# Performance work log

Measured on AMD Instinct MI355X. Metric: run time of the kernel, lower is better.

The kernel has to match this reference:

```python
import jax, jax.numpy as jnp
import numpy as np

N_NODES = 100000
N_EDGES = 3200000
N_FEAT = 128
N_GRAPHS = 256
N_CLASSES = 10


def setup_inputs() -> dict:
    key = jax.random.key(0)
    ks = jax.random.split(key, 10)
    x = jax.random.normal(ks[0], (N_NODES, N_FEAT), dtype=jnp.float32)
    edge_index = jax.random.randint(ks[1], (2, N_EDGES), 0, N_NODES, dtype=jnp.int64)
    batch = jnp.sort(jax.random.randint(ks[2], (N_NODES,), 0, N_GRAPHS, dtype=jnp.int64))
    # GCNConv weights (glorot-ish scaling) and biases
    W1 = jax.random.normal(ks[3], (N_FEAT, 16), dtype=jnp.float32) / np.sqrt(N_FEAT)
    b1 = jnp.zeros((16,), dtype=jnp.float32)
    W2 = jax.random.normal(ks[4], (16, 32), dtype=jnp.float32) / np.sqrt(16.0)
    b2 = jnp.zeros((32,), dtype=jnp.float32)
    Wfc = jax.random.normal(ks[5], (32, N_CLASSES), dtype=jnp.float32) / np.sqrt(32.0)
    bfc = jnp.zeros((N_CLASSES,), dtype=jnp.float32)
    return {"x": x, "edge_index": edge_index, "batch": batch,
            "W1": W1, "b1": b1, "W2": W2, "b2": b2, "Wfc": Wfc, "bfc": bfc}


def reference(x, edge_index, batch, W1, b1, W2, b2, Wfc, bfc):
    N = x.shape[0]
    # --- GCN normalization with self-loops (PyG GCNConv default) ---
    loop = jnp.arange(N, dtype=edge_index.dtype)
    src = jnp.concatenate([edge_index[0], loop])  # [E+N]
    dst = jnp.concatenate([edge_index[1], loop])  # [E+N]
    ones = jnp.ones_like(src, dtype=x.dtype)
    deg = jax.ops.segment_sum(ones, dst, num_segments=N)  # in-degree incl self-loop
    dinv = jax.lax.rsqrt(deg)  # deg >= 1 thanks to self-loops
    norm = dinv[src] * dinv[dst]  # [E+N]

    def gcn_conv(h, W, b):
        h = h @ W                               # [N, out] linear first (small out dim)
        msg = h[src] * norm[:, None]            # gather + edge-wise scale
        agg = jax.ops.segment_sum(msg, dst, num_segments=N)  # scatter-add
        return agg + b

    h = jax.nn.relu(gcn_conv(x, W1, b1))
    h = jax.nn.relu(gcn_conv(h, W2, b2))

    # --- global mean pool over graphs ---
    g_sum = jax.ops.segment_sum(h, batch, num_segments=N_GRAPHS)  # [G, 32]
    g_cnt = jax.ops.segment_sum(jnp.ones((N,), dtype=h.dtype), batch, num_segments=N_GRAPHS)
    pooled = g_sum / jnp.maximum(g_cnt, 1.0)[:, None]

    return pooled @ Wfc + bfc  # [G, num_classes]
```

## Files before the change

kernel.cpp:

```cpp
#include <hip/hip_runtime.h>
#include <hip/hip_fp16.h>

#define NF   128
#define C1   16
#define C2   32
#define NCLS 10
#define BSH  8
#define BN   256
#define MAXB 512
#define S    9216
#define TILE 4096
#define CAP  12288


__global__ __launch_bounds__(512) void k_bin(const int* __restrict__ ei,
                                             int* __restrict__ packed,
                                             int* __restrict__ offmat,
                                             int E, int nbuck) {
    __shared__ int hist[MAXB];
    __shared__ int off0[MAXB];
    __shared__ int cur[MAXB];
    int tid = threadIdx.x;
    long long t0 = (long long)blockIdx.x * TILE;

    for (int i = tid; i < MAXB; i += 512) hist[i] = 0;
    __syncthreads();

    long long eb = t0 + (long long)tid * 8;
    int src[8], dst[8];
    if (eb + 8 <= E) {
        const int4* s4 = (const int4*)(ei + eb);
        const int4* d4 = (const int4*)(ei + E + eb);
        int4 a = s4[0], b = s4[1], c = d4[0], d = d4[1];
        src[0]=a.x; src[1]=a.y; src[2]=a.z; src[3]=a.w;
        src[4]=b.x; src[5]=b.y; src[6]=b.z; src[7]=b.w;
        dst[0]=c.x; dst[1]=c.y; dst[2]=c.z; dst[3]=c.w;
        dst[4]=d.x; dst[5]=d.y; dst[6]=d.z; dst[7]=d.w;
    } else {
#pragma unroll
        for (int u = 0; u < 8; ++u) {
            long long e = eb + u;
            src[u] = (e < E) ? ei[e] : 0;
            dst[u] = (e < E) ? ei[E + e] : -1;
        }
    }
#pragma unroll
    for (int u = 0; u < 8; ++u)
        if (dst[u] >= 0) atomicAdd(&hist[dst[u] >> BSH], 1);
    __syncthreads();
    if (tid < 64) {
        int carry = 0;
        for (int c = 0; c < MAXB / 64; ++c) {
            int idx = c * 64 + tid;
            int v = hist[idx];
            int orig = v;
            for (int off = 1; off < 64; off <<= 1) {
                int t = __shfl_up(v, off);
                if (tid >= off) v += t;
            }
            int ex = v - orig + carry;
            off0[idx] = ex;
            cur[idx] = ex;
            carry += __shfl(v, 63);
        }
    }
    __syncthreads();
    int* orow = offmat + (size_t)blockIdx.x * (nbuck + 1);
    for (int b = tid; b <= nbuck; b += 512) orow[b] = off0[b];
#pragma unroll
    for (int u = 0; u < 8; ++u) {
        int d = dst[u];
        if (d >= 0) {
            int b = d >> BSH;
            int slot = atomicAdd(&cur[b], 1);
            packed[t0 + slot] = src[u] | ((d & (BN - 1)) << 17);
        }
    }
}


__global__ __launch_bounds__(1024) void k_csr(const int* __restrict__ packed,
                                              const int* __restrict__ offmat,
                                              int* __restrict__ csr,
                                              int* __restrict__ rowptr,
                                              int* __restrict__ deg,
                                              float* __restrict__ dinv,
                                              const float* __restrict__ x,
                                              const float* __restrict__ W1,
                                              __half* __restrict__ y1h,
                                              float* __restrict__ g_sum,
                                              int N, int nbuck, int nblkA) {
    __shared__ int stage[CAP];
    __shared__ int startA[1024];
    __shared__ int o1A[1024];
    __shared__ int hcnt[BN];
    __shared__ int cur[BN];
    __shared__ float fdinv[BN];
    __shared__ int wsum[16];
    __shared__ int woff[4];
    int tid = threadIdx.x;
    int wid = tid >> 6, lane = tid & 63;
    int b = blockIdx.x;
    size_t base = (size_t)b * S;

    if (b < 8) g_sum[b * 1024 + tid] = 0.0f;

    int len = 0, o1 = 0;
    if (tid < nblkA) {
        const int* orow = offmat + (size_t)tid * (nbuck + 1) + b;
        o1 = orow[0];
        len = orow[1] - o1;
    }
    o1A[tid] = o1;
    if (tid < BN) hcnt[tid] = 0;

    int v = len;
#pragma unroll
    for (int off = 1; off < 64; off <<= 1) {
        int t = __shfl_up(v, off);
        if (lane >= off) v += t;
    }
    if (lane == 63) wsum[wid] = v;
    __syncthreads();
    if (tid < 16) {
        int w = wsum[tid];
#pragma unroll
        for (int off = 1; off < 16; off <<= 1) {
            int t = __shfl_up(w, off);
            if (tid >= off) w += t;
        }
        wsum[tid] = w;
    }
    __syncthreads();
    int m = wsum[15];
    int incl = v + ((wid > 0) ? wsum[wid - 1] : 0);
    startA[tid] = incl - len;
    __syncthreads();
    if (m > CAP) m = CAP;

    for (int i = tid; i < m; i += 1024) {
        int lo = 0, hi = 1023;
        while (lo < hi) {
            int mid = (lo + hi + 1) >> 1;
            if (startA[mid] <= i) lo = mid; else hi = mid - 1;
        }
        int p = packed[(size_t)lo * TILE + o1A[lo] + (i - startA[lo])];
        stage[i] = p;
        atomicAdd(&hcnt[p >> 17], 1);
    }
    __syncthreads();
    int v2 = (tid < BN) ? hcnt[tid] : 0;
    int s2 = v2;
#pragma unroll
    for (int off = 1; off < 64; off <<= 1) {
        int t = __shfl_up(s2, off);
        if (lane >= off) s2 += t;
    }
    if (tid < BN && lane == 63) wsum[wid] = s2;
    __syncthreads();
    if (tid == 0) {
        int acc = 0;
#pragma unroll
        for (int k = 0; k < 4; ++k) { int t = wsum[k]; woff[k] = acc; acc += t; }
    }
    __syncthreads();
    if (tid < BN) {
        int ex = (s2 - v2) + woff[wid];
        cur[tid] = ex;
        float dv = rsqrtf((float)v2 + 1.0f);
        fdinv[tid] = dv;
        int n = (b << BSH) + tid;
        if (n < N) {
            rowptr[n] = (int)base + ex;
            deg[n] = v2;
            dinv[n] = dv;
        }
    }
    __syncthreads();
    for (int i = tid; i < m; i += 1024) {
        int p = stage[i];
        int slot = atomicAdd(&cur[p >> 17], 1);
        csr[base + slot] = p & 0x1FFFF;
    }
    __syncthreads();

    float* Wl = (float*)stage;
    float* xt = Wl + 2048;
    for (int t = tid; t < NF * C1; t += 1024) Wl[t] = W1[t];
    int n0b = b << BSH;
    const float4* x4 = (const float4*)x;
    for (int iter = 0; iter < 4; ++iter) {
        int r0n = n0b + iter * 64;
        __syncthreads();
        for (int t = tid; t < 64 * 32; t += 1024) {
            int r = t >> 5, c = t & 31;
            int n = r0n + r;
            float4 vv = (n < N) ? x4[(size_t)n * 32 + c] : make_float4(0.f, 0.f, 0.f, 0.f);
            float* dp = &xt[r * 132 + c * 4];
            dp[0] = vv.x; dp[1] = vv.y; dp[2] = vv.z; dp[3] = vv.w;
        }
        __syncthreads();
        int r = tid >> 4, j = tid & 15;
        float acc = 0.0f;
#pragma unroll 4
        for (int k = 0; k < NF; ++k) acc += xt[r * 132 + k] * Wl[k * C1 + j];
        int n = r0n + r;
        if (n < N) y1h[(size_t)n * C1 + j] = __float2half_rn(acc * fdinv[iter * 64 + r]);
    }
}


__global__ __launch_bounds__(256) void k_gather1(const int* __restrict__ rowptr,
                                                 const int* __restrict__ deg,
                                                 const int* __restrict__ csr,
                                                 const float* __restrict__ dinv,
                                                 const float* __restrict__ bias,
                                                 const uint2* __restrict__ yh,
                                                 uint2* __restrict__ outp, int N) {
    int tid = threadIdx.x;
    int j = tid & 3;
    int n = blockIdx.x * 64 + (tid >> 2);
    if (n >= N) return;
    int k0 = rowptr[n];
    int k1 = k0 + deg[n];
    union U { uint2 u; __half2 h[2]; };
    U su; su.u = yh[(size_t)n * 4 + j];
    float2 sl = __half22float2(su.h[0]), shh = __half22float2(su.h[1]);
    float a0 = sl.x, a1 = sl.y, a2 = shh.x, a3 = shh.y;
    float b0 = 0.f, b1v = 0.f, b2 = 0.f, b3 = 0.f;
    int k = k0;
    for (; k + 3 < k1; k += 4) {
        int s0 = csr[k], s1 = csr[k + 1], s2 = csr[k + 2], s3 = csr[k + 3];
        U v0, v1, v2, v3;
        v0.u = yh[(size_t)s0 * 4 + j];
        v1.u = yh[(size_t)s1 * 4 + j];
        v2.u = yh[(size_t)s2 * 4 + j];
        v3.u = yh[(size_t)s3 * 4 + j];
        float2 l0 = __half22float2(v0.h[0]), h0 = __half22float2(v0.h[1]);
        float2 l1 = __half22float2(v1.h[0]), h1 = __half22float2(v1.h[1]);
        float2 l2 = __half22float2(v2.h[0]), h2 = __half22float2(v2.h[1]);
        float2 l3 = __half22float2(v3.h[0]), h3 = __half22float2(v3.h[1]);
        a0 += l0.x; a1 += l0.y; a2 += h0.x; a3 += h0.y;
        b0 += l1.x; b1v += l1.y; b2 += h1.x; b3 += h1.y;
        a0 += l2.x; a1 += l2.y; a2 += h2.x; a3 += h2.y;
        b0 += l3.x; b1v += l3.y; b2 += h3.x; b3 += h3.y;
    }
    for (; k < k1; ++k) {
        U v; v.u = yh[(size_t)csr[k] * 4 + j];
        float2 l = __half22float2(v.h[0]), h = __half22float2(v.h[1]);
        a0 += l.x; a1 += l.y; a2 += h.x; a3 += h.y;
    }
    float dn = dinv[n];
    float r0 = dn * (a0 + b0), r1 = dn * (a1 + b1v);
    float r2 = dn * (a2 + b2), r3 = dn * (a3 + b3);
    float4 bb = ((const float4*)bias)[j];
    U o;
    o.h[0] = __floats2half2_rn(fmaxf(r0 + bb.x, 0.0f) * dn, fmaxf(r1 + bb.y, 0.0f) * dn);
    o.h[1] = __floats2half2_rn(fmaxf(r2 + bb.z, 0.0f) * dn, fmaxf(r3 + bb.w, 0.0f) * dn);
    outp[(size_t)n * 4 + j] = o.u;
}


__global__ __launch_bounds__(256) void k_gather_pool(const int* __restrict__ rowptr,
                                                     const int* __restrict__ deg,
                                                     const int* __restrict__ csr,
                                                     const float* __restrict__ dinv,
                                                     const float* __restrict__ W2,
                                                     const float* __restrict__ b2,
                                                     const int* __restrict__ batch,
                                                     const uint2* __restrict__ yh,
                                                     float* __restrict__ g_sum, int N) {
    __shared__ float W2s[C1 * C2];
    __shared__ float acc[64 * C2];
    int tid = threadIdx.x;
    for (int t = tid; t < C1 * C2; t += 256) W2s[t] = W2[t];
    for (int t = tid; t < 64 * C2; t += 256) acc[t] = 0.0f;

    int n0 = blockIdx.x * 64;
    int g_lo = batch[min(n0, N - 1)];
    int g_hi = batch[min(n0 + 63, N - 1)];
    __syncthreads();

    int j = tid & 3;
    int n = n0 + (tid >> 2);
    if (n < N) {
        int k0 = rowptr[n];
        int k1 = k0 + deg[n];
        union U { uint2 u; __half2 h[2]; };
        U su; su.u = yh[(size_t)n * 4 + j];
        float2 sl = __half22float2(su.h[0]), shh = __half22float2(su.h[1]);
        float a0 = sl.x, a1 = sl.y, a2 = shh.x, a3 = shh.y;
        float b0 = 0.f, b1v = 0.f, b2v = 0.f, b3 = 0.f;
        int k = k0;
        for (; k + 3 < k1; k += 4) {
            int s0 = csr[k], s1 = csr[k + 1], s2 = csr[k + 2], s3 = csr[k + 3];
            U v0, v1, v2, v3;
            v0.u = yh[(size_t)s0 * 4 + j];
            v1.u = yh[(size_t)s1 * 4 + j];
            v2.u = yh[(size_t)s2 * 4 + j];
            v3.u = yh[(size_t)s3 * 4 + j];
            float2 l0 = __half22float2(v0.h[0]), h0 = __half22float2(v0.h[1]);
            float2 l1 = __half22float2(v1.h[0]), h1 = __half22float2(v1.h[1]);
            float2 l2 = __half22float2(v2.h[0]), h2 = __half22float2(v2.h[1]);
            float2 l3 = __half22float2(v3.h[0]), h3 = __half22float2(v3.h[1]);
            a0 += l0.x; a1 += l0.y; a2 += h0.x; a3 += h0.y;
            b0 += l1.x; b1v += l1.y; b2v += h1.x; b3 += h1.y;
            a0 += l2.x; a1 += l2.y; a2 += h2.x; a3 += h2.y;
            b0 += l3.x; b1v += l3.y; b2v += h3.x; b3 += h3.y;
        }
        for (; k < k1; ++k) {
            U v; v.u = yh[(size_t)csr[k] * 4 + j];
            float2 l = __half22float2(v.h[0]), h = __half22float2(v.h[1]);
            a0 += l.x; a1 += l.y; a2 += h.x; a3 += h.y;
        }
        float dn = dinv[n];
        float z0 = dn * (a0 + b0), z1 = dn * (a1 + b1v);
        float z2 = dn * (a2 + b2v), z3 = dn * (a3 + b3);

        float p[C2];
        const float* w0 = &W2s[(4 * j + 0) * C2];
        const float* w1 = &W2s[(4 * j + 1) * C2];
        const float* w2 = &W2s[(4 * j + 2) * C2];
        const float* w3 = &W2s[(4 * j + 3) * C2];
#pragma unroll
        for (int i = 0; i < C2; ++i)
            p[i] = z0 * w0[i] + z1 * w1[i] + z2 * w2[i] + z3 * w3[i];
#pragma unroll
        for (int i = 0; i < C2; ++i) {
            p[i] += __shfl_xor(p[i], 1);
            p[i] += __shfl_xor(p[i], 2);
        }
        int g = batch[n];
        float* arow = &acc[(g - g_lo) * C2];
#pragma unroll
        for (int i = 0; i < 8; ++i) {
            int c = j * 8 + i;
            atomicAdd(&arow[c], fmaxf(p[c] + b2[c], 0.0f));
        }
    }
    __syncthreads();
    int nslots = g_hi - g_lo + 1;
    for (int t = tid; t < nslots * C2; t += 256) {
        int s = t >> 5, c = t & 31;
        float v = acc[s * C2 + c];
        if (v != 0.0f) atomicAdd(&g_sum[(size_t)(g_lo + s) * C2 + c], v);
    }
}


__global__ __launch_bounds__(256) void k_final(const float* __restrict__ g_sum,
                                               const int* __restrict__ batch,
                                               const float* __restrict__ Wfc,
                                               const float* __restrict__ bfc,
                                               float* __restrict__ out, int N, int G) {
    int g = threadIdx.x;
    if (g >= G) return;
    int lo = 0, hi = N;
    while (lo < hi) { int m = (lo + hi) >> 1; if (batch[m] < g) lo = m + 1; else hi = m; }
    int start = lo;
    lo = start; hi = N;
    while (lo < hi) { int m = (lo + hi) >> 1; if (batch[m] < g + 1) lo = m + 1; else hi = m; }
    float inv = 1.0f / fmaxf((float)(lo - start), 1.0f);
    float pooled[C2];
#pragma unroll
    for (int jj = 0; jj < C2; ++jj) pooled[jj] = g_sum[(size_t)g * C2 + jj] * inv;
#pragma unroll
    for (int c = 0; c < NCLS; ++c) {
        float a = bfc[c];
#pragma unroll
        for (int jj = 0; jj < C2; ++jj) a += pooled[jj] * Wfc[jj * NCLS + c];
        out[g * NCLS + c] = a;
    }
}

extern "C" void kernel_launch(void* const* d_in, const int* in_sizes, int n_in,
                              void* d_out, int out_size, void* d_ws, size_t ws_size,
                              hipStream_t stream) {
    const float* x    = (const float*)d_in[0];
    const int*   ei   = (const int*)d_in[1];
    const int*   batch= (const int*)d_in[2];
    const float* W1   = (const float*)d_in[3];
    const float* b1   = (const float*)d_in[4];
    const float* W2   = (const float*)d_in[5];
    const float* b2   = (const float*)d_in[6];
    const float* Wfc  = (const float*)d_in[7];
    const float* bfc  = (const float*)d_in[8];
    float* out = (float*)d_out;

    const int N = in_sizes[0] / NF;
    const int E = in_sizes[1] / 2;
    const int G = out_size / NCLS;
    const int nbuck = (N + BN - 1) >> BSH;
    const int nblkA = (E + TILE - 1) / TILE;

    char* p = (char*)d_ws;
    auto alloc = [&](size_t bytes) { char* q = p; p += (bytes + 63) & ~(size_t)63; return q; };
    int*     rowptr  = (int*)    alloc((size_t)N * 4);
    int*     deg     = (int*)    alloc((size_t)N * 4);
    float*   dinv    = (float*)  alloc((size_t)N * 4);
    int*     packed  = (int*)    alloc((size_t)nblkA * TILE * 4);
    int*     offmat  = (int*)    alloc((size_t)nblkA * (nbuck + 1) * 4);
    int*     csr     = (int*)    alloc((size_t)nbuck * S * 4);
    __half*  y1h     = (__half*) alloc((size_t)N * C1 * 2);
    __half*  uh      = (__half*) alloc((size_t)N * C1 * 2);
    float*   g_sum   = (float*)  alloc((size_t)G * C2 * 4);

    k_bin<<<nblkA, 512, 0, stream>>>(ei, packed, offmat, E, nbuck);
    k_csr<<<nbuck, 1024, 0, stream>>>(packed, offmat, csr, rowptr, deg, dinv,
                                      x, W1, y1h, g_sum, N, nbuck, nblkA);

    k_gather1<<<(N + 63) / 64, 256, 0, stream>>>(rowptr, deg, csr, dinv, b1,
                                                 (const uint2*)y1h, (uint2*)uh, N);
    k_gather_pool<<<(N + 63) / 64, 256, 0, stream>>>(rowptr, deg, csr, dinv, W2, b2,
                                                     batch, (const uint2*)uh, g_sum, N);
    k_final<<<1, 256, 0, stream>>>(g_sum, batch, Wfc, bfc, out, N, G);
}
```

Measured before the change: 176.7 us.

## Split first-layer linear transform out of CSR build into separate kernel

Moves the x@W1 projection (scaled by dinv, stored as fp16) out of the CSR construction kernel into its own k_lin1 kernel, which uses 256-thread blocks of 16 rows each and far more blocks. The g_sum zeroing becomes a hipMemsetAsync. The aim is to stop the 391-block CSR kernel from serialising a 51MB read of x behind its scatter phase, and to spread that read over many more workgroups for better bandwidth. In exchange it adds two launches and a global read of dinv instead of a shared-memory value.

```diff
diff --git a/kernel.cpp b/kernel.cpp
--- a/kernel.cpp
+++ b/kernel.cpp
@@ -85,17 +85,12 @@
                                               int* __restrict__ rowptr,
                                               int* __restrict__ deg,
                                               float* __restrict__ dinv,
-                                              const float* __restrict__ x,
-                                              const float* __restrict__ W1,
-                                              __half* __restrict__ y1h,
-                                              float* __restrict__ g_sum,
                                               int N, int nbuck, int nblkA) {
     __shared__ int stage[CAP];
     __shared__ int startA[1024];
     __shared__ int o1A[1024];
     __shared__ int hcnt[BN];
     __shared__ int cur[BN];
-    __shared__ float fdinv[BN];
     __shared__ int wsum[16];
     __shared__ int woff[4];
     int tid = threadIdx.x;
@@ -103,8 +98,6 @@
     int b = blockIdx.x;
     size_t base = (size_t)b * S;
 
-    if (b < 8) g_sum[b * 1024 + tid] = 0.0f;
-
     int len = 0, o1 = 0;
     if (tid < nblkA) {
         const int* orow = offmat + (size_t)tid * (nbuck + 1) + b;
@@ -167,13 +160,11 @@
     if (tid < BN) {
         int ex = (s2 - v2) + woff[wid];
         cur[tid] = ex;
-        float dv = rsqrtf((float)v2 + 1.0f);
-        fdinv[tid] = dv;
         int n = (b << BSH) + tid;
         if (n < N) {
             rowptr[n] = (int)base + ex;
             deg[n] = v2;
-            dinv[n] = dv;
+            dinv[n] = rsqrtf((float)v2 + 1.0f);
         }
     }
     __syncthreads();
@@ -182,31 +173,33 @@
         int slot = atomicAdd(&cur[p >> 17], 1);
         csr[base + slot] = p & 0x1FFFF;
     }
-    __syncthreads();
-
-    float* Wl = (float*)stage;
-    float* xt = Wl + 2048;
-    for (int t = tid; t < NF * C1; t += 1024) Wl[t] = W1[t];
-    int n0b = b << BSH;
+}
+
+
+__global__ __launch_bounds__(256) void k_lin1(const float* __restrict__ x,
+                                              const float* __restrict__ W1,
+                                              const float* __restrict__ dinv,
+                                              __half* __restrict__ y1h, int N) {
+    __shared__ float ws[NF * C1];
+    __shared__ float xs[16 * 132];
+    int tid = threadIdx.x;
+    for (int t = tid; t < NF * C1; t += 256) ws[t] = W1[t];
+    int n0 = blockIdx.x * 16;
     const float4* x4 = (const float4*)x;
-    for (int iter = 0; iter < 4; ++iter) {
-        int r0n = n0b + iter * 64;
-        __syncthreads();
-        for (int t = tid; t < 64 * 32; t += 1024) {
-            int r = t >> 5, c = t & 31;
-            int n = r0n + r;
-            float4 vv = (n < N) ? x4[(size_t)n * 32 + c] : make_float4(0.f, 0.f, 0.f, 0.f);
-            float* dp = &xt[r * 132 + c * 4];
-            dp[0] = vv.x; dp[1] = vv.y; dp[2] = vv.z; dp[3] = vv.w;
-        }
-        __syncthreads();
-        int r = tid >> 4, j = tid & 15;
-        float acc = 0.0f;
+    for (int t = tid; t < 16 * 32; t += 256) {
+        int r = t >> 5, c = t & 31;
+        int n = n0 + r;
+        float4 v = (n < N) ? x4[(size_t)n * 32 + c] : make_float4(0.f, 0.f, 0.f, 0.f);
+        float* d = &xs[r * 132 + c * 4];
+        d[0] = v.x; d[1] = v.y; d[2] = v.z; d[3] = v.w;
+    }
+    __syncthreads();
+    int r = tid >> 4, j = tid & 15;
+    float acc = 0.0f;
 #pragma unroll 4
-        for (int k = 0; k < NF; ++k) acc += xt[r * 132 + k] * Wl[k * C1 + j];
-        int n = r0n + r;
-        if (n < N) y1h[(size_t)n * C1 + j] = __float2half_rn(acc * fdinv[iter * 64 + r]);
-    }
+    for (int k = 0; k < NF; ++k) acc += xs[r * 132 + k] * ws[k * C1 + j];
+    int n = n0 + r;
+    if (n < N) y1h[(size_t)n * C1 + j] = __float2half_rn(acc * dinv[n]);
 }
 
 
@@ -406,9 +399,11 @@
     float*   g_sum   = (float*)  alloc((size_t)G * C2 * 4);
 
     k_bin<<<nblkA, 512, 0, stream>>>(ei, packed, offmat, E, nbuck);
+    hipMemsetAsync(g_sum, 0, (size_t)G * C2 * 4, stream);
     k_csr<<<nbuck, 1024, 0, stream>>>(packed, offmat, csr, rowptr, deg, dinv,
-                                      x, W1, y1h, g_sum, N, nbuck, nblkA);
-
+                                      N, nbuck, nblkA);
+
+    k_lin1<<<(N + 15) / 16, 256, 0, stream>>>(x, W1, dinv, y1h, N);
     k_gather1<<<(N + 63) / 64, 256, 0, stream>>>(rowptr, deg, csr, dinv, b1,
                                                  (const uint2*)y1h, (uint2*)uh, N);
     k_gather_pool<<<(N + 63) / 64, 256, 0, stream>>>(rowptr, deg, csr, dinv, W2, b2,
```

Measured after the change: 179.3 us. No clear change (+1.5%).
